# Performance work log

Hardware: AMD Instinct MI355X
Metric: run time of the kernel (lower is better)

## Reference

```python
import jax, jax.numpy as jnp
import numpy as np

D_MODEL = 1024
N_HEADS = 16
D_K = D_MODEL // N_HEADS
B, L = 4, 2048


def setup_inputs() -> dict:
    key = jax.random.key(0)
    ks = jax.random.split(key, 9)
    s = 1.0 / np.sqrt(D_MODEL)
    return {
        "x": jax.random.normal(ks[0], (B, L, D_MODEL), dtype=jnp.float32),
        "mask": jnp.ones((B, L), dtype=jnp.int32),
        "Wq": jax.random.uniform(ks[1], (D_MODEL, D_MODEL), jnp.float32, -s, s),
        "bq": jax.random.uniform(ks[2], (D_MODEL,), jnp.float32, -s, s),
        "Wk": jax.random.uniform(ks[3], (D_MODEL, D_MODEL), jnp.float32, -s, s),
        "bk": jax.random.uniform(ks[4], (D_MODEL,), jnp.float32, -s, s),
        "Wv": jax.random.uniform(ks[5], (D_MODEL, D_MODEL), jnp.float32, -s, s),
        "bv": jax.random.uniform(ks[6], (D_MODEL,), jnp.float32, -s, s),
        "Wo": jax.random.uniform(ks[7], (D_MODEL, D_MODEL), jnp.float32, -s, s),
        "bo": jax.random.uniform(ks[8], (D_MODEL,), jnp.float32, -s, s),
    }


def reference(x, mask, Wq, bq, Wk, bk, Wv, bv, Wo, bo):
    b, l, d = x.shape
    # project and split heads: [B, H, L, d_k]
    def heads(W, bias):
        return (x @ W.T + bias).reshape(b, l, N_HEADS, D_K).transpose(0, 2, 1, 3)
    Q = heads(Wq, bq)
    K = heads(Wk, bk)
    V = heads(Wv, bv)
    scores = jnp.einsum("bhqd,bhkd->bhqk", Q, K) / np.sqrt(D_K).astype(np.float32)
    # mask: [B, L] -> broadcast over heads and query dim as [B, 1, 1, L]
    scores = jnp.where(mask[:, None, None, :] == 0, jnp.float32(-1e9), scores)
    attn = jax.nn.softmax(scores, axis=-1)  # dropout=0 in eval math
    out = jnp.einsum("bhqk,bhkd->bhqd", attn, V)
    out = out.transpose(0, 2, 1, 3).reshape(b, l, d)
    return out @ Wo.T + bo
```

## Files before the change

### kernel.cpp

```cpp
#include <hip/hip_runtime.h>
#include <stdint.h>

#define DMODEL 1024
#define NHEADS 16
#define DK     64
#define BATCH  4
#define SEQ    2048
#define MROWS  (BATCH*SEQ)

typedef __bf16 bf16x8 __attribute__((ext_vector_type(8)));
typedef float  f32x4  __attribute__((ext_vector_type(4)));

#if defined(__has_builtin)
#if __has_builtin(__builtin_amdgcn_exp2f)
#define EXP2F(x) __builtin_amdgcn_exp2f(x)
#endif
#endif
#ifndef EXP2F
#define EXP2F(x) exp2f(x)
#endif

__device__ __forceinline__ unsigned short f2bf(float f) {
    unsigned int u = __builtin_bit_cast(unsigned int, f);
    u += 0x7fffu + ((u >> 16) & 1u);
    return (unsigned short)(u >> 16);
}

__device__ __forceinline__ unsigned int pack_bf16(float a, float b) {
    unsigned int ua = __builtin_bit_cast(unsigned int, a) + 0x8000u;
    unsigned int ub = __builtin_bit_cast(unsigned int, b) + 0x8000u;
    return __builtin_amdgcn_perm(ub, ua, 0x07060302u);
}

#define GLDS(gp, lp) __builtin_amdgcn_global_load_lds( \
    (const __attribute__((address_space(1))) unsigned int*)(gp), \
    (__attribute__((address_space(3))) unsigned int*)(lp), 16, 0, 0)

__global__ void cvt_kernel(const float* __restrict__ src,
                           unsigned short* __restrict__ dst, int n4) {
    int i = blockIdx.x * blockDim.x + threadIdx.x;
    if (i >= n4) return;
    const float4 v = reinterpret_cast<const float4*>(src)[i];
    ushort4 o;
    o.x = f2bf(v.x); o.y = f2bf(v.y); o.z = f2bf(v.z); o.w = f2bf(v.w);
    reinterpret_cast<ushort4*>(dst)[i] = o;
}

__global__ void cvtw_kernel(const float* __restrict__ w0, const float* __restrict__ w1,
                            const float* __restrict__ w2, const float* __restrict__ w3,
                            unsigned short* __restrict__ d0, unsigned short* __restrict__ d1,
                            unsigned short* __restrict__ d2, unsigned short* __restrict__ d3) {
    const float* s; unsigned short* d;
    switch (blockIdx.y) {
        case 0:  s = w0; d = d0; break;
        case 1:  s = w1; d = d1; break;
        case 2:  s = w2; d = d2; break;
        default: s = w3; d = d3; break;
    }
    const int i = blockIdx.x * blockDim.x + threadIdx.x;
    const float4 v = reinterpret_cast<const float4*>(s)[i];
    ushort4 o;
    o.x = f2bf(v.x); o.y = f2bf(v.y); o.z = f2bf(v.z); o.w = f2bf(v.w);
    reinterpret_cast<ushort4*>(d)[i] = o;
}

__global__ void maskbias_kernel(const int* __restrict__ m, float* __restrict__ o, int n) {
    const int i = blockIdx.x * blockDim.x + threadIdx.x;
    if (i < n) o[i] = m[i] ? 0.f : -1e30f;
}

template<int MODE>
__global__ __launch_bounds__(256, 3) void gemm128(
        const unsigned short* __restrict__ A,
        const unsigned short* __restrict__ W0,
        const unsigned short* __restrict__ W1,
        const unsigned short* __restrict__ W2,
        const float* __restrict__ b0,
        const float* __restrict__ b1,
        const float* __restrict__ b2,
        void* __restrict__ o0, void* __restrict__ o1, void* __restrict__ o2) {
    __shared__ unsigned short As[128 * 64];
    __shared__ unsigned short Bs[128 * 64];
    const int lane = threadIdx.x & 63;
    const int wave = threadIdx.x >> 6;
    const int quad = lane >> 4;
    const int r15  = lane & 15;
    const int wr = wave >> 1, wc = wave & 1;
    const int m0 = blockIdx.y * 128;

    int which, ncol0;
    const unsigned short* W;
    const float* bias;
    if (MODE == 0) {
        which = blockIdx.x >> 3;
        ncol0 = (blockIdx.x & 7) * 128;
        W    = which == 0 ? W0 : (which == 1 ? W1 : W2);
        bias = which == 0 ? b0 : (which == 1 ? b1 : b2);
    } else {
        which = 0; ncol0 = blockIdx.x * 128; W = W0; bias = b0;
    }

    const int srow = lane >> 3;
    const int scg  = (lane & 7) ^ srow;
    const unsigned short* Ag[4];
    const unsigned short* Wg[4];
    #pragma unroll
    for (int j = 0; j < 4; ++j) {
        const int row = (wave * 4 + j) * 8 + srow;
        Ag[j] = A + (m0 + row) * DMODEL + scg * 8;
        Wg[j] = W + (ncol0 + row) * DMODEL + scg * 8;
    }

    f32x4 acc[4][4] = {};
    for (int kk = 0; kk < DMODEL; kk += 64) {
        __syncthreads();
        #pragma unroll
        for (int j = 0; j < 4; ++j) {
            GLDS(Ag[j] + kk, &As[(wave * 4 + j) * 512]);
            GLDS(Wg[j] + kk, &Bs[(wave * 4 + j) * 512]);
        }
        __syncthreads();
        #pragma unroll
        for (int u = 0; u < 2; ++u) {
            bf16x8 af[4], bfx[4];
            const int cs = ((u * 4 + quad) ^ (r15 & 7)) * 8;
            #pragma unroll
            for (int t = 0; t < 4; ++t) {
                af[t]  = *(const bf16x8*)&As[(wr * 64 + t * 16 + r15) * 64 + cs];
                bfx[t] = *(const bf16x8*)&Bs[(wc * 64 + t * 16 + r15) * 64 + cs];
            }
            #pragma unroll
            for (int mt = 0; mt < 4; ++mt)
                #pragma unroll
                for (int nt = 0; nt < 4; ++nt)
                    acc[mt][nt] = __builtin_amdgcn_mfma_f32_16x16x32_bf16(
                        af[mt], bfx[nt], acc[mt][nt], 0, 0, 0);
        }
    }

    #pragma unroll
    for (int mt = 0; mt < 4; ++mt) {
        #pragma unroll
        for (int nt = 0; nt < 4; ++nt) {
            #pragma unroll
            for (int r = 0; r < 4; ++r) {
                const int row = m0 + wr * 64 + mt * 16 + quad * 4 + r;
                const int col = ncol0 + wc * 64 + nt * 16 + r15;
                float v = acc[mt][nt][r] + bias[col];
                if (MODE == 1) {
                    ((float*)o0)[(size_t)row * DMODEL + col] = v;
                } else {
                    if (which == 0) v *= 0.18033688011112042f;
                    const int b = row >> 11, l = row & (SEQ - 1);
                    const int h = col >> 6,  d = col & (DK - 1);
                    const int bh = b * NHEADS + h;
                    unsigned short* ow = (unsigned short*)(which == 0 ? o0 : (which == 1 ? o1 : o2));
                    size_t idx;
                    if (which < 2) idx = ((size_t)bh * SEQ + l) * DK + d;
                    else           idx = (size_t)bh * (SEQ * DK) + (l >> 6) * (DK * 64) + d * 64 + (l & 63);
                    ow[idx] = f2bf(v);
                }
            }
        }
    }
}

__global__ __launch_bounds__(256, 4) void flash_attn(
        const unsigned short* __restrict__ Q,
        const unsigned short* __restrict__ Km,
        const unsigned short* __restrict__ Vm,
        const float* __restrict__ mbf,
        unsigned short* __restrict__ Oa) {
    __shared__ unsigned short Ks[2][64 * 64];
    __shared__ unsigned short Vs[64 * 64];
    __shared__ unsigned short Pl[4][2][16 * 64];
    const int lane = threadIdx.x & 63;
    const int wave = threadIdx.x >> 6;
    const int quad = lane >> 4;
    const int r15  = lane & 15;

    const int id   = (blockIdx.y << 4) | blockIdx.x;
    const int xcd  = id & 7;
    const int slot = id >> 3;
    const int bh   = xcd + ((slot >> 4) << 3);
    const int qt   = slot & 15;
    const int b = bh >> 4, h = bh & (NHEADS - 1);
    const int q0 = qt * 128 + wave * 32;

    const unsigned short* Qb = Q  + (size_t)bh * SEQ * DK;
    const unsigned short* Kb = Km + (size_t)bh * SEQ * DK;
    const unsigned short* Vb = Vm + (size_t)bh * SEQ * DK;
    const float* mb = mbf + b * SEQ;

    const int srow = lane >> 3;
    const int soff = ((lane >> 3) * 64) + (((lane & 7) ^ srow) * 8);

    bf16x8 bq[2][2];
    #pragma unroll
    for (int qf = 0; qf < 2; ++qf)
        #pragma unroll
        for (int u = 0; u < 2; ++u)
            bq[qf][u] = *(const bf16x8*)(Qb + (q0 + qf * 16 + r15) * DK + u * 32 + quad * 8);

    float l_part[2] = {0.f, 0.f};
    f32x4 oacc[2][4] = {};

    #pragma unroll
    for (int j = 0; j < 2; ++j) {
        const int wseg = wave * 2 + j;
        GLDS(Kb + wseg * 512 + soff, &Ks[0][wseg * 512]);
        GLDS(Vb + wseg * 512 + soff, &Vs[wseg * 512]);
    }
    __syncthreads();

    #define NT (SEQ / 64)
    for (int t = 0; t < NT; ++t) {
        const int kb = t * 64;
        const int cur = t & 1;

        float4 m4v[4];
        #pragma unroll
        for (int tt = 0; tt < 4; ++tt)
            m4v[tt] = *(const float4*)(mb + kb + tt * 16 + quad * 4);

        if (t + 1 < NT) {
            const unsigned short* Kg = Kb + (kb + 64) * 64;
            #pragma unroll
            for (int j = 0; j < 2; ++j) {
                const int wseg = wave * 2 + j;
                GLDS(Kg + wseg * 512 + soff, &Ks[cur ^ 1][wseg * 512]);
            }
        }

        char* const Pb = (char*)&Pl[wave][0][0];
        #pragma unroll
        for (int tt = 0; tt < 4; ++tt) {
            const bf16x8 ak0 = *(const bf16x8*)&Ks[cur][(tt * 16 + r15) * 64 + ((quad ^ (r15 & 7)) * 8)];
            const bf16x8 ak1 = *(const bf16x8*)&Ks[cur][(tt * 16 + r15) * 64 + (((4 + quad) ^ (r15 & 7)) * 8)];
            const float4 m4 = m4v[tt];
            #pragma unroll
            for (int qf = 0; qf < 2; ++qf) {
                f32x4 z = {};
                z = __builtin_amdgcn_mfma_f32_16x16x32_bf16(ak0, bq[qf][0], z, 0, 0, 0);
                z = __builtin_amdgcn_mfma_f32_16x16x32_bf16(ak1, bq[qf][1], z, 0, 0, 0);
                const float p0 = EXP2F(z[0] + m4.x);
                const float p1 = EXP2F(z[1] + m4.y);
                const float p2 = EXP2F(z[2] + m4.z);
                const float p3 = EXP2F(z[3] + m4.w);
                l_part[qf] += (p0 + p1) + (p2 + p3);
                uint2 pw;
                pw.x = pack_bf16(p0, p1);
                pw.y = pack_bf16(p2, p3);
                const int c2 = (tt * 2 + (quad >> 1)) ^ (r15 & 7);
                *(uint2*)(Pb + qf * 2048 + r15 * 128 + c2 * 16 + (quad & 1) * 8) = pw;
            }
        }

        __syncthreads();

        #pragma unroll
        for (int u = 0; u < 2; ++u) {
            const int cs = ((u * 4 + quad) ^ (r15 & 7)) * 8;
            bf16x8 vf[4];
            #pragma unroll
            for (int nt = 0; nt < 4; ++nt)
                vf[nt] = *(const bf16x8*)&Vs[(nt * 16 + r15) * 64 + cs];
            #pragma unroll
            for (int qf = 0; qf < 2; ++qf) {
                const bf16x8 ap = *(const bf16x8*)(Pb + qf * 2048 + r15 * 128 + cs * 2);
                #pragma unroll
                for (int nt = 0; nt < 4; ++nt)
                    oacc[qf][nt] = __builtin_amdgcn_mfma_f32_16x16x32_bf16(
                        ap, vf[nt], oacc[qf][nt], 0, 0, 0);
            }
        }

        __syncthreads();

        if (t + 1 < NT) {
            const unsigned short* Vg = Vb + (kb + 64) * 64;
            #pragma unroll
            for (int j = 0; j < 2; ++j) {
                const int wseg = wave * 2 + j;
                GLDS(Vg + wseg * 512 + soff, &Vs[wseg * 512]);
            }
        }
    }
    #undef NT

    #pragma unroll
    for (int qf = 0; qf < 2; ++qf) {
        float l = l_part[qf];
        l += __shfl_xor(l, 16);
        l += __shfl_xor(l, 32);
        float lq[4];
        #pragma unroll
        for (int r = 0; r < 4; ++r) lq[r] = __shfl(l, quad * 4 + r, 64);
        #pragma unroll
        for (int nt = 0; nt < 4; ++nt) {
            #pragma unroll
            for (int r = 0; r < 4; ++r) {
                const int row = q0 + qf * 16 + quad * 4 + r;
                const int col = h * DK + nt * 16 + r15;
                Oa[((size_t)b * SEQ + row) * DMODEL + col] = f2bf(oacc[qf][nt][r] / lq[r]);
            }
        }
    }
}

extern "C" void kernel_launch(void* const* d_in, const int* in_sizes, int n_in,
                              void* d_out, int out_size, void* d_ws, size_t ws_size,
                              hipStream_t stream) {
    (void)in_sizes; (void)n_in; (void)out_size; (void)ws_size;
    const float* x  = (const float*)d_in[0];
    const int* mask = (const int*)d_in[1];
    const float* Wq = (const float*)d_in[2];
    const float* bq = (const float*)d_in[3];
    const float* Wk = (const float*)d_in[4];
    const float* bk = (const float*)d_in[5];
    const float* Wv = (const float*)d_in[6];
    const float* bv = (const float*)d_in[7];
    const float* Wo = (const float*)d_in[8];
    const float* bo = (const float*)d_in[9];
    float* out = (float*)d_out;

    char* ws = (char*)d_ws;
    unsigned short* xb  = (unsigned short*)(ws);
    unsigned short* wqb = (unsigned short*)(ws + 16777216);
    unsigned short* wkb = (unsigned short*)(ws + 16777216 + 1 * 2097152);
    unsigned short* wvb = (unsigned short*)(ws + 16777216 + 2 * 2097152);
    unsigned short* wob = (unsigned short*)(ws + 16777216 + 3 * 2097152);
    unsigned short* qb  = (unsigned short*)(ws + 16777216 + 4 * 2097152);
    unsigned short* kb  = qb  + (size_t)MROWS * DMODEL;
    unsigned short* vtb = kb  + (size_t)MROWS * DMODEL;
    unsigned short* ab  = vtb + (size_t)MROWS * DMODEL;
    float*          mbf = (float*)(ab + (size_t)MROWS * DMODEL);

    cvt_kernel<<<dim3(MROWS * DMODEL / 4 / 256), 256, 0, stream>>>(x, xb, MROWS * DMODEL / 4);
    cvtw_kernel<<<dim3(DMODEL * DMODEL / 4 / 256, 4), 256, 0, stream>>>(
        Wq, Wk, Wv, Wo, wqb, wkb, wvb, wob);
    maskbias_kernel<<<dim3(BATCH * SEQ / 256), 256, 0, stream>>>(mask, mbf, BATCH * SEQ);

    gemm128<0><<<dim3(24, MROWS / 128), 256, 0, stream>>>(
        xb, wqb, wkb, wvb, bq, bk, bv, qb, kb, vtb);

    flash_attn<<<dim3(16, BATCH * NHEADS), 256, 0, stream>>>(qb, kb, vtb, mbf, ab);

    gemm128<1><<<dim3(8, MROWS / 128), 256, 0, stream>>>(
        ab, wob, nullptr, nullptr, bo, nullptr, nullptr, out, nullptr, nullptr);
}
```

Measured before the change: 312.5 us.

## Double-buffer GEMM LDS tiles with 256x128 blocks and raise PV MFMA priority

The projection GEMMs move to 512-thread blocks covering 256x128 output tiles. They use two LDS buffers so the global-to-LDS load of the next K slice overlaps the MFMA work on the current one, replacing two barriers per iteration with one. The flash-attention P·V MFMA section is wrapped in s_setprio to favour matrix work. The larger LDS footprint (96KB) and launch bound of one block per CU reduce occupancy and halve the grid size, so latency hiding depends more on the explicit prefetch.

```diff
diff --git a/kernel.cpp b/kernel.cpp
--- a/kernel.cpp
+++ b/kernel.cpp
@@ -70,7 +70,7 @@
 }
 
 template<int MODE>
-__global__ __launch_bounds__(256, 3) void gemm128(
+__global__ __launch_bounds__(512, 1) void gemm256(
         const unsigned short* __restrict__ A,
         const unsigned short* __restrict__ W0,
         const unsigned short* __restrict__ W1,
@@ -79,14 +79,15 @@
         const float* __restrict__ b1,
         const float* __restrict__ b2,
         void* __restrict__ o0, void* __restrict__ o1, void* __restrict__ o2) {
-    __shared__ unsigned short As[128 * 64];
-    __shared__ unsigned short Bs[128 * 64];
-    const int lane = threadIdx.x & 63;
-    const int wave = threadIdx.x >> 6;
+    __shared__ unsigned short As[2][256 * 64];
+    __shared__ unsigned short Bs[2][128 * 64];
+    const int tid  = threadIdx.x;
+    const int lane = tid & 63;
+    const int wave = tid >> 6;
     const int quad = lane >> 4;
     const int r15  = lane & 15;
     const int wr = wave >> 1, wc = wave & 1;
-    const int m0 = blockIdx.y * 128;
+    const int m0 = blockIdx.y * 256;
 
     int which, ncol0;
     const unsigned short* W;
@@ -103,31 +104,40 @@
     const int srow = lane >> 3;
     const int scg  = (lane & 7) ^ srow;
     const unsigned short* Ag[4];
-    const unsigned short* Wg[4];
-    #pragma unroll
-    for (int j = 0; j < 4; ++j) {
-        const int row = (wave * 4 + j) * 8 + srow;
-        Ag[j] = A + (m0 + row) * DMODEL + scg * 8;
-        Wg[j] = W + (ncol0 + row) * DMODEL + scg * 8;
-    }
+    const unsigned short* Wg[2];
+    #pragma unroll
+    for (int j = 0; j < 4; ++j)
+        Ag[j] = A + (size_t)(m0 + j * 64 + wave * 8 + srow) * DMODEL + scg * 8;
+    #pragma unroll
+    for (int j = 0; j < 2; ++j)
+        Wg[j] = W + (size_t)(ncol0 + j * 64 + wave * 8 + srow) * DMODEL + scg * 8;
 
     f32x4 acc[4][4] = {};
+
+    #pragma unroll
+    for (int j = 0; j < 4; ++j) GLDS(Ag[j], &As[0][(j * 64 + wave * 8) * 64]);
+    #pragma unroll
+    for (int j = 0; j < 2; ++j) GLDS(Wg[j], &Bs[0][(j * 64 + wave * 8) * 64]);
+    __syncthreads();
+
+    int buf = 0;
     for (int kk = 0; kk < DMODEL; kk += 64) {
-        __syncthreads();
-        #pragma unroll
-        for (int j = 0; j < 4; ++j) {
-            GLDS(Ag[j] + kk, &As[(wave * 4 + j) * 512]);
-            GLDS(Wg[j] + kk, &Bs[(wave * 4 + j) * 512]);
-        }
-        __syncthreads();
+        if (kk + 64 < DMODEL) {
+            #pragma unroll
+            for (int j = 0; j < 4; ++j)
+                GLDS(Ag[j] + kk + 64, &As[buf ^ 1][(j * 64 + wave * 8) * 64]);
+            #pragma unroll
+            for (int j = 0; j < 2; ++j)
+                GLDS(Wg[j] + kk + 64, &Bs[buf ^ 1][(j * 64 + wave * 8) * 64]);
+        }
         #pragma unroll
         for (int u = 0; u < 2; ++u) {
             bf16x8 af[4], bfx[4];
             const int cs = ((u * 4 + quad) ^ (r15 & 7)) * 8;
             #pragma unroll
             for (int t = 0; t < 4; ++t) {
-                af[t]  = *(const bf16x8*)&As[(wr * 64 + t * 16 + r15) * 64 + cs];
-                bfx[t] = *(const bf16x8*)&Bs[(wc * 64 + t * 16 + r15) * 64 + cs];
+                af[t]  = *(const bf16x8*)&As[buf][(wr * 64 + t * 16 + r15) * 64 + cs];
+                bfx[t] = *(const bf16x8*)&Bs[buf][(wc * 64 + t * 16 + r15) * 64 + cs];
             }
             #pragma unroll
             for (int mt = 0; mt < 4; ++mt)
@@ -136,6 +146,8 @@
                     acc[mt][nt] = __builtin_amdgcn_mfma_f32_16x16x32_bf16(
                         af[mt], bfx[nt], acc[mt][nt], 0, 0, 0);
         }
+        __syncthreads();
+        buf ^= 1;
     }
 
     #pragma unroll
@@ -258,6 +270,7 @@
 
         __syncthreads();
 
+        __builtin_amdgcn_s_setprio(1);
         #pragma unroll
         for (int u = 0; u < 2; ++u) {
             const int cs = ((u * 4 + quad) ^ (r15 & 7)) * 8;
@@ -274,6 +287,7 @@
                         ap, vf[nt], oacc[qf][nt], 0, 0, 0);
             }
         }
+        __builtin_amdgcn_s_setprio(0);
 
         __syncthreads();
 
@@ -341,11 +355,11 @@
         Wq, Wk, Wv, Wo, wqb, wkb, wvb, wob);
     maskbias_kernel<<<dim3(BATCH * SEQ / 256), 256, 0, stream>>>(mask, mbf, BATCH * SEQ);
 
-    gemm128<0><<<dim3(24, MROWS / 128), 256, 0, stream>>>(
+    gemm256<0><<<dim3(24, MROWS / 256), 512, 0, stream>>>(
         xb, wqb, wkb, wvb, bq, bk, bv, qb, kb, vtb);
 
     flash_attn<<<dim3(16, BATCH * NHEADS), 256, 0, stream>>>(qb, kb, vtb, mbf, ab);
 
-    gemm128<1><<<dim3(8, MROWS / 128), 256, 0, stream>>>(
+    gemm256<1><<<dim3(8, MROWS / 256), 512, 0, stream>>>(
         ab, wob, nullptr, nullptr, bo, nullptr, nullptr, out, nullptr, nullptr);
 }
```

After: 318.6 us. About the same (+2.0%).
